# Performance work log

Hardware: AMD Instinct MI355X
Metric: run time of the kernel (lower is better)

## Reference

```python
import jax, jax.numpy as jnp
import numpy as np

N = 1_000_000   # active voxels
CIN = 32
COUT = 64
K = 9           # 3x3 kernel offsets (rulebook size)
EPS = 1e-5


def setup_inputs() -> dict:
    key = jax.random.key(0)
    ks = jax.random.split(key, 6)
    x = jax.random.normal(ks[0], (N, CIN), dtype=jnp.float32)
    # rulebook: neighbor index per (voxel, kernel offset); stride=1 so same coord set
    nbr = jax.random.randint(ks[1], (N, K), 0, N, dtype=jnp.int32)
    W1 = jax.random.normal(ks[2], (K, CIN, COUT), dtype=jnp.float32) * (1.0 / np.sqrt(K * CIN))
    W2 = jax.random.normal(ks[3], (K, COUT, COUT), dtype=jnp.float32) * (1.0 / np.sqrt(K * COUT))
    Wd = jax.random.normal(ks[4], (CIN, COUT), dtype=jnp.float32) * (1.0 / np.sqrt(CIN))
    g1 = jnp.ones((COUT,), jnp.float32); b1 = jnp.zeros((COUT,), jnp.float32)
    g2 = jnp.ones((COUT,), jnp.float32); b2 = jnp.zeros((COUT,), jnp.float32)
    gd = jnp.ones((COUT,), jnp.float32); bd = jnp.zeros((COUT,), jnp.float32)
    return {"x": x, "W1": W1, "g1": g1, "b1": b1, "W2": W2, "g2": g2, "b2": b2,
            "Wd": Wd, "gd": gd, "bd": bd, "nbr": nbr}


def _sparse_conv(x, nbr, W):
    # gather-GEMM-scatter; loop over the fixed K=9 kernel offsets to avoid
    # materializing the full [N, K, Cin] gathered tensor
    out = jnp.zeros((x.shape[0], W.shape[-1]), dtype=x.dtype)
    for k in range(W.shape[0]):
        out = out + jnp.take(x, nbr[:, k], axis=0) @ W[k]
    return out


def _bn(x, gamma, beta):
    # BatchNorm1d over the voxel dimension (training-mode batch statistics)
    mu = jnp.mean(x, axis=0)
    var = jnp.var(x, axis=0)
    return gamma * (x - mu) * jax.lax.rsqrt(var + EPS) + beta


def reference(x, W1, g1, b1, W2, g2, b2, Wd, gd, bd, nbr):
    # downsample branch (1x1 conv -> BN, no relu) since in_ch != out_ch
    identity = _bn(x @ Wd, gd, bd)
    # conv1: SparseConv3x3 -> BN -> ReLU
    out = jax.nn.relu(_bn(_sparse_conv(x, nbr, W1), g1, b1))
    # conv2: SparseConv3x3 -> BN (no relu)
    out = _bn(_sparse_conv(out, nbr, W2), g2, b2)
    # residual add + final ReLU
    return jax.nn.relu(out + identity)
```

## Files before the change

kernel.cpp:

```cpp
#include <hip/hip_runtime.h>
#include <hip/hip_bf16.h>

#define NV 1000000
#define CI 32
#define CO 64
#define KK 9
#define NG (NV / 16)
#define EPSV 1e-5f

typedef __bf16 bf16x8 __attribute__((ext_vector_type(8)));
typedef float  f32x4  __attribute__((ext_vector_type(4)));

__device__ __forceinline__ f32x4 mfma16(bf16x8 a, bf16x8 b, f32x4 c) {
    return __builtin_amdgcn_mfma_f32_16x16x32_bf16(a, b, c, 0, 0, 0);
}

__device__ __forceinline__ float xredseg(float v) {
    v += __shfl_xor(v, 16, 64);
    v += __shfl_xor(v, 32, 64);
    return v;
}

__global__ void k_prep_w(const float* __restrict__ W1, const float* __restrict__ W2,
                         const float* __restrict__ Wd,
                         __bf16* __restrict__ W1T, __bf16* __restrict__ W2T,
                         __bf16* __restrict__ WdT) {
    int i = blockIdx.x * blockDim.x + threadIdx.x;
    const int n1 = KK * CO * CI;
    const int n2 = KK * CO * CO;
    const int nd = CO * CI;
    if (i < n1) {
        int k = i / (CO * CI), r = i % (CO * CI), co = r / CI, ci = r % CI;
        W1T[i] = (__bf16)W1[(k * CI + ci) * CO + co];
    } else if (i < n1 + n2) {
        int j = i - n1;
        int k = j / (CO * CO), r = j % (CO * CO), co = r / CO, ci = r % CO;
        W2T[j] = (__bf16)W2[(k * CO + ci) * CO + co];
    } else if (i < n1 + n2 + nd) {
        int j = i - n1 - n2;
        int co = j / CI, ci = j % CI;
        WdT[j] = (__bf16)Wd[ci * CO + co];
    }
}

__global__ void k_prep_x(const float* __restrict__ x, __bf16* __restrict__ xb) {
    int i = blockIdx.x * blockDim.x + threadIdx.x;
    const float4* px = (const float4*)x + 2 * (size_t)i;
    float4 u = px[0], v = px[1];
    bf16x8 o;
    o[0] = (__bf16)u.x; o[1] = (__bf16)u.y; o[2] = (__bf16)u.z; o[3] = (__bf16)u.w;
    o[4] = (__bf16)v.x; o[5] = (__bf16)v.y; o[6] = (__bf16)v.z; o[7] = (__bf16)v.w;
    *((bf16x8*)xb + i) = o;
}

__global__ __launch_bounds__(256, 2) void k_conv1(
    const __bf16* __restrict__ xb, const int* __restrict__ nbr,
    const __bf16* __restrict__ W1T, const __bf16* __restrict__ WdT,
    __bf16* __restrict__ y1b, float* __restrict__ stats) {
    const int lane = threadIdx.x & 63;
    const int w    = threadIdx.x >> 6;
    const int r    = lane & 15;
    const int seg  = lane >> 4;

    bf16x8 w1[KK][4];
#pragma unroll
    for (int k = 0; k < KK; k++)
#pragma unroll
        for (int t = 0; t < 4; t++)
            w1[k][t] = *(const bf16x8*)(W1T + ((size_t)(k * CO + t * 16 + r)) * CI + seg * 8);
    bf16x8 wd[4];
#pragma unroll
    for (int t = 0; t < 4; t++)
        wd[t] = *(const bf16x8*)(WdT + (size_t)(t * 16 + r) * CI + seg * 8);

    float ps1[4] = {0.f,0.f,0.f,0.f}, pq1[4] = {0.f,0.f,0.f,0.f};
    float psd[4] = {0.f,0.f,0.f,0.f}, pqd[4] = {0.f,0.f,0.f,0.f};

    const int slot = blockIdx.x * 4 + w;
    const int nslots = gridDim.x * 4;
    const f32x4 z = {0.f, 0.f, 0.f, 0.f};

    for (int gid = slot; gid < NG; gid += nslots) {
        const int vb = gid * 16;
        const int v  = vb + r;
        const long nb = (long)v * KK;

        int idxs[KK];
#pragma unroll
        for (int k = 0; k < KK; k++) idxs[k] = nbr[nb + k];

        f32x4 acc[4]  = {z, z, z, z};
        f32x4 accd[4] = {z, z, z, z};

        bf16x8 ad = *(const bf16x8*)(xb + (size_t)v * CI + seg * 8);
#pragma unroll
        for (int t = 0; t < 4; t++) accd[t] = mfma16(ad, wd[t], accd[t]);

#pragma unroll
        for (int k = 0; k < KK; k++) {
            bf16x8 a = *(const bf16x8*)(xb + (size_t)idxs[k] * CI + seg * 8);
#pragma unroll
            for (int t = 0; t < 4; t++) acc[t] = mfma16(a, w1[k][t], acc[t]);
        }

#pragma unroll
        for (int t = 0; t < 4; t++) {
#pragma unroll
            for (int rr = 0; rr < 4; rr++) {
                float val = acc[t][rr];
                int row = vb + seg * 4 + rr;
                __builtin_nontemporal_store((__bf16)val, &y1b[(size_t)row * CO + t * 16 + r]);
                ps1[t] += val; pq1[t] += val * val;
                float dv = accd[t][rr];
                psd[t] += dv; pqd[t] += dv * dv;
            }
        }
    }

#pragma unroll
    for (int t = 0; t < 4; t++) {
        ps1[t] = xredseg(ps1[t]); pq1[t] = xredseg(pq1[t]);
        psd[t] = xredseg(psd[t]); pqd[t] = xredseg(pqd[t]);
    }
    if (lane < 16) {
#pragma unroll
        for (int t = 0; t < 4; t++) {
            atomicAdd(&stats[0 * 64 + t * 16 + lane], ps1[t]);
            atomicAdd(&stats[1 * 64 + t * 16 + lane], pq1[t]);
            atomicAdd(&stats[2 * 64 + t * 16 + lane], psd[t]);
            atomicAdd(&stats[3 * 64 + t * 16 + lane], pqd[t]);
        }
    }
}

__global__ void k_bnrelu(__bf16* __restrict__ y1b, const float* __restrict__ stats,
                         const float* __restrict__ g1, const float* __restrict__ b1) {
    __shared__ float sc[CO], sh[CO];
    int t = threadIdx.x;
    if (t < CO) {
        float mu  = stats[0 * 64 + t] * (1.0f / NV);
        float var = stats[1 * 64 + t] * (1.0f / NV) - mu * mu;
        float s = g1[t] * rsqrtf(var + EPSV);
        sc[t] = s; sh[t] = b1[t] - mu * s;
    }
    __syncthreads();
    size_t i = (size_t)blockIdx.x * blockDim.x + threadIdx.x;
    bf16x8* p = (bf16x8*)y1b + i;
    bf16x8 vv = *p;
    int c0 = 8 * ((int)(i & 7));
    bf16x8 o;
#pragma unroll
    for (int j = 0; j < 8; j++) {
        float f = (float)vv[j];
        f = sc[c0 + j] * f + sh[c0 + j];
        o[j] = (__bf16)fmaxf(f, 0.f);
    }
    *p = o;
}

#define TILE_B (16 * KK * 128)

__global__ __launch_bounds__(128, 2) void k_conv2(
    const __bf16* __restrict__ h1b, const int* __restrict__ nbr,
    const __bf16* __restrict__ W2T,
    float* __restrict__ y2, float* __restrict__ stats) {
    __shared__ __align__(16) char smem[2][TILE_B];

    const int lane = threadIdx.x & 63;
    const int w    = threadIdx.x >> 6;
    const int r    = lane & 15;
    const int seg  = lane >> 4;

    bf16x8 w2[KK][2][2];
#pragma unroll
    for (int k = 0; k < KK; k++)
#pragma unroll
        for (int t2 = 0; t2 < 2; t2++)
#pragma unroll
            for (int s = 0; s < 2; s++) {
                int co = w * 32 + t2 * 16 + r;
                int ci = s * 32 + seg * 8;
                w2[k][t2][s] = *(const bf16x8*)(W2T + ((size_t)(k * CO + co)) * CO + ci);
            }

    float ps[2] = {0.f, 0.f}, pq[2] = {0.f, 0.f};
    const f32x4 z = {0.f, 0.f, 0.f, 0.f};
    const int sw = r & 7;

    auto stage = [&](char* buf, int it) {
        const int* nb = nbr + (size_t)it * (16 * KK);
#pragma unroll
        for (int s = 0; s < 9; s++) {
            int c = w * 576 + s * 64 + lane;
            int ruleIdx = c >> 3;
            int i = (ruleIdx * 57) >> 9;
            int p = (c & 7) ^ (i & 7);
            int idx = nb[ruleIdx];
            const __bf16* src = h1b + (size_t)idx * CO + p * 8;
            __builtin_amdgcn_global_load_lds(
                (const __attribute__((address_space(1))) void*)src,
                (__attribute__((address_space(3))) void*)(buf + w * 9216 + s * 1024),
                16, 0, 0);
        }
    };

    int it = blockIdx.x;
    int cur = 0;
    if (it < NG) stage(smem[0], it);
    __syncthreads();

    for (; it < NG; it += gridDim.x) {
        int nxt = it + gridDim.x;
        if (nxt < NG) stage(smem[cur ^ 1], nxt);

        const __bf16* base = (const __bf16*)smem[cur];
        f32x4 acc[2] = {z, z};
#pragma unroll
        for (int k = 0; k < KK; k++) {
            const __bf16* rp = base + (size_t)(r * KK + k) * 64;
            bf16x8 a0 = *(const bf16x8*)(rp + ((seg ^ sw) * 8));
            bf16x8 a1 = *(const bf16x8*)(rp + (((4 + seg) ^ sw) * 8));
            acc[0] = mfma16(a0, w2[k][0][0], acc[0]);
            acc[0] = mfma16(a1, w2[k][0][1], acc[0]);
            acc[1] = mfma16(a0, w2[k][1][0], acc[1]);
            acc[1] = mfma16(a1, w2[k][1][1], acc[1]);
        }

        const int vb = it * 16;
#pragma unroll
        for (int t2 = 0; t2 < 2; t2++) {
#pragma unroll
            for (int rr = 0; rr < 4; rr++) {
                float val = acc[t2][rr];
                int row = vb + seg * 4 + rr;
                int c = w * 32 + t2 * 16 + r;
                __builtin_nontemporal_store(val, &y2[(size_t)row * CO + c]);
                ps[t2] += val; pq[t2] += val * val;
            }
        }

        __syncthreads();
        cur ^= 1;
    }

#pragma unroll
    for (int t2 = 0; t2 < 2; t2++) { ps[t2] = xredseg(ps[t2]); pq[t2] = xredseg(pq[t2]); }
    if (lane < 16) {
#pragma unroll
        for (int t2 = 0; t2 < 2; t2++) {
            atomicAdd(&stats[4 * 64 + w * 32 + t2 * 16 + lane], ps[t2]);
            atomicAdd(&stats[5 * 64 + w * 32 + t2 * 16 + lane], pq[t2]);
        }
    }
}

__global__ __launch_bounds__(256, 2) void k_final(
    const __bf16* __restrict__ xb, const __bf16* __restrict__ WdT,
    float* __restrict__ out, const float* __restrict__ stats,
    const float* __restrict__ g2, const float* __restrict__ b2,
    const float* __restrict__ gd, const float* __restrict__ bd) {
    __shared__ float s2[CO], sh2[CO], sdv[CO], shd[CO];
    int t = threadIdx.x;
    if (t < CO) {
        float mu2  = stats[4 * 64 + t] * (1.0f / NV);
        float var2 = stats[5 * 64 + t] * (1.0f / NV) - mu2 * mu2;
        float s = g2[t] * rsqrtf(var2 + EPSV);
        s2[t] = s; sh2[t] = b2[t] - mu2 * s;
        float mud  = stats[2 * 64 + t] * (1.0f / NV);
        float vard = stats[3 * 64 + t] * (1.0f / NV) - mud * mud;
        float sd = gd[t] * rsqrtf(vard + EPSV);
        sdv[t] = sd; shd[t] = bd[t] - mud * sd;
    }
    __syncthreads();

    const int lane = threadIdx.x & 63;
    const int w    = threadIdx.x >> 6;
    const int r    = lane & 15;
    const int seg  = lane >> 4;

    bf16x8 wd[4];
#pragma unroll
    for (int t4 = 0; t4 < 4; t4++)
        wd[t4] = *(const bf16x8*)(WdT + (size_t)(t4 * 16 + r) * CI + seg * 8);

    const int slot = blockIdx.x * 4 + w;
    const int nslots = gridDim.x * 4;
    const f32x4 z = {0.f, 0.f, 0.f, 0.f};

    for (int gid = slot; gid < NG; gid += nslots) {
        const int vb = gid * 16;
        const int v  = vb + r;
        bf16x8 ad = *(const bf16x8*)(xb + (size_t)v * CI + seg * 8);
        f32x4 accd[4] = {z, z, z, z};
#pragma unroll
        for (int t4 = 0; t4 < 4; t4++) accd[t4] = mfma16(ad, wd[t4], accd[t4]);
#pragma unroll
        for (int t4 = 0; t4 < 4; t4++) {
#pragma unroll
            for (int rr = 0; rr < 4; rr++) {
                int row = vb + seg * 4 + rr;
                int c = t4 * 16 + r;
                size_t o = (size_t)row * CO + c;
                float y2v = out[o];
                float res = s2[c] * y2v + sh2[c] + sdv[c] * accd[t4][rr] + shd[c];
                out[o] = fmaxf(res, 0.f);
            }
        }
    }
}

extern "C" void kernel_launch(void* const* d_in, const int* in_sizes, int n_in,
                              void* d_out, int out_size, void* d_ws, size_t ws_size,
                              hipStream_t stream) {
    const float* x  = (const float*)d_in[0];
    const float* W1 = (const float*)d_in[1];
    const float* g1 = (const float*)d_in[2];
    const float* b1 = (const float*)d_in[3];
    const float* W2 = (const float*)d_in[4];
    const float* g2 = (const float*)d_in[5];
    const float* b2 = (const float*)d_in[6];
    const float* Wd = (const float*)d_in[7];
    const float* gd = (const float*)d_in[8];
    const float* bd = (const float*)d_in[9];
    const int*  nbr = (const int*)d_in[10];

    char* ws = (char*)d_ws;
    __bf16* xb  = (__bf16*)ws;
    __bf16* y1b = (__bf16*)(ws + 64000000);
    __bf16* W1T = (__bf16*)(ws + 192000000);
    __bf16* W2T = W1T + KK * CO * CI;
    __bf16* WdT = W2T + KK * CO * CO;
    float* stats = (float*)(ws + 192000000 + 2 * (KK*CO*CI + KK*CO*CO + CO*CI));

    hipMemsetAsync(stats, 0, 6 * 64 * sizeof(float), stream);

    int nprep = KK*CO*CI + KK*CO*CO + CO*CI;
    k_prep_w<<<(nprep + 255) / 256, 256, 0, stream>>>(W1, W2, Wd, W1T, W2T, WdT);
    k_prep_x<<<(NV * CI / 8) / 256, 256, 0, stream>>>(x, xb);
    k_conv1<<<1024, 256, 0, stream>>>(xb, nbr, W1T, WdT, y1b, stats);
    k_bnrelu<<<(NV * CO / 8) / 256, 256, 0, stream>>>(y1b, stats, g1, b1);
    k_conv2<<<1024, 128, 0, stream>>>(y1b, nbr, W2T, (float*)d_out, stats);
    k_final<<<1024, 256, 0, stream>>>(xb, WdT, (float*)d_out, stats, g2, b2, gd, bd);
}
```

Baseline: 634.3 us.

## Double-buffer conv1 neighbor gathers into LDS with async global_load_lds

conv1 now gathers neighbor feature rows with asynchronous global-to-LDS loads into a per-wave double buffer. Neighbor indices for the next group are prefetched one step further ahead, and manual vmcnt waits replace the implicit dependency stalls. The goal is to overlap the random-access gather latency with the MFMA work on the current group. The kernel uses more LDS (about 72KB per block) and the grid is halved to 512 blocks. The hand-counted vmcnt thresholds make correctness depend on exactly how many memory instructions are in flight.

```diff
diff --git a/kernel.cpp b/kernel.cpp
--- a/kernel.cpp
+++ b/kernel.cpp
@@ -57,10 +57,14 @@
     const __bf16* __restrict__ xb, const int* __restrict__ nbr,
     const __bf16* __restrict__ W1T, const __bf16* __restrict__ WdT,
     __bf16* __restrict__ y1b, float* __restrict__ stats) {
+    __shared__ __align__(16) char smem[4][2][KK * 1024];
+
     const int lane = threadIdx.x & 63;
     const int w    = threadIdx.x >> 6;
     const int r    = lane & 15;
     const int seg  = lane >> 4;
+    const int rq   = lane >> 2;
+    const int part = lane & 3;
 
     bf16x8 w1[KK][4];
 #pragma unroll
@@ -76,29 +80,60 @@
     float ps1[4] = {0.f,0.f,0.f,0.f}, pq1[4] = {0.f,0.f,0.f,0.f};
     float psd[4] = {0.f,0.f,0.f,0.f}, pqd[4] = {0.f,0.f,0.f,0.f};
 
-    const int slot = blockIdx.x * 4 + w;
-    const int nslots = gridDim.x * 4;
+    const int slot   = blockIdx.x * 4 + w;
+    const int stride = gridDim.x * 4;
     const f32x4 z = {0.f, 0.f, 0.f, 0.f};
 
-    for (int gid = slot; gid < NG; gid += nslots) {
-        const int vb = gid * 16;
-        const int v  = vb + r;
-        const long nb = (long)v * KK;
-
-        int idxs[KK];
-#pragma unroll
-        for (int k = 0; k < KK; k++) idxs[k] = nbr[nb + k];
+    int idxs[KK];
+    auto load_idx = [&](int it) {
+        const volatile int* nb = nbr + (size_t)it * (16 * KK) + rq * KK;
+#pragma unroll
+        for (int k = 0; k < KK; k++) idxs[k] = nb[k];
+    };
+    auto stage = [&](int buf) {
+        char* dst = smem[w][buf];
+#pragma unroll
+        for (int k = 0; k < KK; k++) {
+            const __bf16* src = xb + (size_t)idxs[k] * CI + part * 8;
+            __builtin_amdgcn_global_load_lds(
+                (const __attribute__((address_space(1))) void*)src,
+                (__attribute__((address_space(3))) void*)(dst + k * 1024),
+                16, 0, 0);
+        }
+    };
+
+    int it  = slot;
+    load_idx(it);
+    stage(0);
+    int nxt = it + stride;
+    if (nxt < NG) load_idx(nxt);
+    int cur = 0;
+
+    while (true) {
+        const int nxt2 = nxt + stride;
+        if (nxt < NG) {
+            stage(cur ^ 1);
+            if (nxt2 < NG) load_idx(nxt2);
+        }
+        __builtin_amdgcn_sched_barrier(0);
+        if (nxt2 < NG)      asm volatile("s_waitcnt vmcnt(18)" ::: "memory");
+        else if (nxt < NG)  asm volatile("s_waitcnt vmcnt(9)"  ::: "memory");
+        else                asm volatile("s_waitcnt vmcnt(0)"  ::: "memory");
+        __builtin_amdgcn_sched_barrier(0);
+
+        const __bf16* base = (const __bf16*)smem[w][cur];
+        const int vb = it * 16;
 
         f32x4 acc[4]  = {z, z, z, z};
         f32x4 accd[4] = {z, z, z, z};
 
-        bf16x8 ad = *(const bf16x8*)(xb + (size_t)v * CI + seg * 8);
+        bf16x8 ad = *(const bf16x8*)(xb + (size_t)(vb + r) * CI + seg * 8);
 #pragma unroll
         for (int t = 0; t < 4; t++) accd[t] = mfma16(ad, wd[t], accd[t]);
 
 #pragma unroll
         for (int k = 0; k < KK; k++) {
-            bf16x8 a = *(const bf16x8*)(xb + (size_t)idxs[k] * CI + seg * 8);
+            bf16x8 a = *(const bf16x8*)(base + k * 512 + r * 32 + seg * 8);
 #pragma unroll
             for (int t = 0; t < 4; t++) acc[t] = mfma16(a, w1[k][t], acc[t]);
         }
@@ -115,6 +150,9 @@
                 psd[t] += dv; pqd[t] += dv * dv;
             }
         }
+
+        if (nxt >= NG) break;
+        it = nxt; nxt = nxt2; cur ^= 1;
     }
 
 #pragma unroll
@@ -337,7 +375,7 @@
     int nprep = KK*CO*CI + KK*CO*CO + CO*CI;
     k_prep_w<<<(nprep + 255) / 256, 256, 0, stream>>>(W1, W2, Wd, W1T, W2T, WdT);
     k_prep_x<<<(NV * CI / 8) / 256, 256, 0, stream>>>(x, xb);
-    k_conv1<<<1024, 256, 0, stream>>>(xb, nbr, W1T, WdT, y1b, stats);
+    k_conv1<<<512, 256, 0, stream>>>(xb, nbr, W1T, WdT, y1b, stats);
     k_bnrelu<<<(NV * CO / 8) / 256, 256, 0, stream>>>(y1b, stats, g1, b1);
     k_conv2<<<1024, 128, 0, stream>>>(y1b, nbr, W2T, (float*)d_out, stats);
     k_final<<<1024, 256, 0, stream>>>(xb, WdT, (float*)d_out, stats, g2, b2, gd, bd);
```

New measurement: 682.7 us. +7.6%, slower.

## Fuse BN+ReLU into conv2 gather and software-pipeline conv1 gathers with LDS weights

Applied to the files above, without the earlier changes.

Removes the separate BN+ReLU pass over y1 by applying the scale/shift and ReLU to each gathered neighbor row inside conv2 before the MFMA. This eliminates a full read and write of the intermediate, at the cost of repeating the elementwise work nine times per row in conv2. Conv1 now keeps W1 in LDS instead of registers and double-buffers the neighbor index loads and gathers across tiles to overlap memory latency with MFMA work. The conv1 grid is reduced to 768 blocks.

```diff
diff --git a/kernel.cpp b/kernel.cpp
--- a/kernel.cpp
+++ b/kernel.cpp
@@ -57,17 +57,23 @@
     const __bf16* __restrict__ xb, const int* __restrict__ nbr,
     const __bf16* __restrict__ W1T, const __bf16* __restrict__ WdT,
     __bf16* __restrict__ y1b, float* __restrict__ stats) {
+    __shared__ __align__(16) char w1smem[KK * CO * CI * 2];
+
     const int lane = threadIdx.x & 63;
     const int w    = threadIdx.x >> 6;
     const int r    = lane & 15;
     const int seg  = lane >> 4;
 
-    bf16x8 w1[KK][4];
-#pragma unroll
-    for (int k = 0; k < KK; k++)
-#pragma unroll
-        for (int t = 0; t < 4; t++)
-            w1[k][t] = *(const bf16x8*)(W1T + ((size_t)(k * CO + t * 16 + r)) * CI + seg * 8);
+#pragma unroll
+    for (int j = 0; j < 9; j++) {
+        const __bf16* srcp = W1T + (size_t)(j * 256 + threadIdx.x) * 8;
+        __builtin_amdgcn_global_load_lds(
+            (const __attribute__((address_space(1))) void*)srcp,
+            (__attribute__((address_space(3))) void*)(w1smem + j * 4096 + w * 1024),
+            16, 0, 0);
+    }
+    __syncthreads();
+
     bf16x8 wd[4];
 #pragma unroll
     for (int t = 0; t < 4; t++)
@@ -76,33 +82,42 @@
     float ps1[4] = {0.f,0.f,0.f,0.f}, pq1[4] = {0.f,0.f,0.f,0.f};
     float psd[4] = {0.f,0.f,0.f,0.f}, pqd[4] = {0.f,0.f,0.f,0.f};
 
-    const int slot = blockIdx.x * 4 + w;
-    const int nslots = gridDim.x * 4;
+    const int slot   = blockIdx.x * 4 + w;
+    const int stride = gridDim.x * 4;
     const f32x4 z = {0.f, 0.f, 0.f, 0.f};
 
-    for (int gid = slot; gid < NG; gid += nslots) {
-        const int vb = gid * 16;
-        const int v  = vb + r;
-        const long nb = (long)v * KK;
-
-        int idxs[KK];
-#pragma unroll
-        for (int k = 0; k < KK; k++) idxs[k] = nbr[nb + k];
+    auto loadIdx = [&](int (&idx)[KK], int tile) {
+        const int* nb = nbr + (size_t)(tile * 16 + r) * KK;
+#pragma unroll
+        for (int k = 0; k < KK; k++) idx[k] = nb[k];
+    };
+    auto gather9 = [&](bf16x8 (&g)[KK], const int (&idx)[KK]) {
+#pragma unroll
+        for (int k = 0; k < KK; k++)
+            g[k] = *(const bf16x8*)(xb + (size_t)idx[k] * CI + seg * 8);
+    };
+    auto loadAd = [&](int tile) {
+        return *(const bf16x8*)(xb + (size_t)(tile * 16 + r) * CI + seg * 8);
+    };
+    auto compute = [&](int tile, const bf16x8 (&g)[KK], bf16x8 ad) {
+        int w1off = 0;
+        asm volatile("" : "+v"(w1off));
+        const __bf16* wb = (const __bf16*)w1smem + w1off;
 
         f32x4 acc[4]  = {z, z, z, z};
         f32x4 accd[4] = {z, z, z, z};
-
-        bf16x8 ad = *(const bf16x8*)(xb + (size_t)v * CI + seg * 8);
 #pragma unroll
         for (int t = 0; t < 4; t++) accd[t] = mfma16(ad, wd[t], accd[t]);
-
 #pragma unroll
         for (int k = 0; k < KK; k++) {
-            bf16x8 a = *(const bf16x8*)(xb + (size_t)idxs[k] * CI + seg * 8);
-#pragma unroll
-            for (int t = 0; t < 4; t++) acc[t] = mfma16(a, w1[k][t], acc[t]);
-        }
-
+#pragma unroll
+            for (int t = 0; t < 4; t++) {
+                bf16x8 b = *(const bf16x8*)(wb + k * 2048 + t * 512 + r * 32 + seg * 8);
+                acc[t] = mfma16(g[k], b, acc[t]);
+            }
+        }
+
+        const int vb = tile * 16;
 #pragma unroll
         for (int t = 0; t < 4; t++) {
 #pragma unroll
@@ -115,6 +130,37 @@
                 psd[t] += dv; pqd[t] += dv * dv;
             }
         }
+    };
+
+    int idx0[KK], idx1[KK];
+    bf16x8 g0[KK], g1[KK];
+    bf16x8 ad0, ad1;
+
+    int it = slot;
+    loadIdx(idx0, it);
+    gather9(g0, idx0); ad0 = loadAd(it);
+    int itn = it + stride;
+    bool have = (itn < NG);
+    if (have) loadIdx(idx1, itn);
+
+    while (true) {
+        if (have) {
+            gather9(g1, idx1); ad1 = loadAd(itn);
+            int it2 = itn + stride;
+            if (it2 < NG) loadIdx(idx0, it2);
+        }
+        compute(it, g0, ad0);
+        if (!have) break;
+        it = itn; itn = it + stride; have = (itn < NG);
+
+        if (have) {
+            gather9(g0, idx0); ad0 = loadAd(itn);
+            int it2 = itn + stride;
+            if (it2 < NG) loadIdx(idx1, it2);
+        }
+        compute(it, g1, ad1);
+        if (!have) break;
+        it = itn; itn = it + stride; have = (itn < NG);
     }
 
 #pragma unroll
@@ -133,36 +179,12 @@
     }
 }
 
-__global__ void k_bnrelu(__bf16* __restrict__ y1b, const float* __restrict__ stats,
-                         const float* __restrict__ g1, const float* __restrict__ b1) {
-    __shared__ float sc[CO], sh[CO];
-    int t = threadIdx.x;
-    if (t < CO) {
-        float mu  = stats[0 * 64 + t] * (1.0f / NV);
-        float var = stats[1 * 64 + t] * (1.0f / NV) - mu * mu;
-        float s = g1[t] * rsqrtf(var + EPSV);
-        sc[t] = s; sh[t] = b1[t] - mu * s;
-    }
-    __syncthreads();
-    size_t i = (size_t)blockIdx.x * blockDim.x + threadIdx.x;
-    bf16x8* p = (bf16x8*)y1b + i;
-    bf16x8 vv = *p;
-    int c0 = 8 * ((int)(i & 7));
-    bf16x8 o;
-#pragma unroll
-    for (int j = 0; j < 8; j++) {
-        float f = (float)vv[j];
-        f = sc[c0 + j] * f + sh[c0 + j];
-        o[j] = (__bf16)fmaxf(f, 0.f);
-    }
-    *p = o;
-}
-
 #define TILE_B (16 * KK * 128)
 
 __global__ __launch_bounds__(128, 2) void k_conv2(
     const __bf16* __restrict__ h1b, const int* __restrict__ nbr,
-    const __bf16* __restrict__ W2T,
+    const __bf16* __restrict__ W2T, const float* __restrict__ g1,
+    const float* __restrict__ b1,
     float* __restrict__ y2, float* __restrict__ stats) {
     __shared__ __align__(16) char smem[2][TILE_B];
 
@@ -182,6 +204,21 @@
                 int ci = s * 32 + seg * 8;
                 w2[k][t2][s] = *(const bf16x8*)(W2T + ((size_t)(k * CO + co)) * CO + ci);
             }
+
+    float scA[8], shA[8], scB[8], shB[8];
+#pragma unroll
+    for (int j = 0; j < 8; j++) {
+        int cA = seg * 8 + j;
+        float muA = stats[cA] * (1.0f / NV);
+        float vaA = stats[64 + cA] * (1.0f / NV) - muA * muA;
+        float sA  = g1[cA] * rsqrtf(vaA + EPSV);
+        scA[j] = sA; shA[j] = b1[cA] - muA * sA;
+        int cB = 32 + seg * 8 + j;
+        float muB = stats[cB] * (1.0f / NV);
+        float vaB = stats[64 + cB] * (1.0f / NV) - muB * muB;
+        float sB  = g1[cB] * rsqrtf(vaB + EPSV);
+        scB[j] = sB; shB[j] = b1[cB] - muB * sB;
+    }
 
     float ps[2] = {0.f, 0.f}, pq[2] = {0.f, 0.f};
     const f32x4 z = {0.f, 0.f, 0.f, 0.f};
@@ -218,8 +255,14 @@
 #pragma unroll
         for (int k = 0; k < KK; k++) {
             const __bf16* rp = base + (size_t)(r * KK + k) * 64;
-            bf16x8 a0 = *(const bf16x8*)(rp + ((seg ^ sw) * 8));
-            bf16x8 a1 = *(const bf16x8*)(rp + (((4 + seg) ^ sw) * 8));
+            bf16x8 a0r = *(const bf16x8*)(rp + ((seg ^ sw) * 8));
+            bf16x8 a1r = *(const bf16x8*)(rp + (((4 + seg) ^ sw) * 8));
+            bf16x8 a0, a1;
+#pragma unroll
+            for (int j = 0; j < 8; j++) {
+                a0[j] = (__bf16)fmaxf((float)a0r[j] * scA[j] + shA[j], 0.f);
+                a1[j] = (__bf16)fmaxf((float)a1r[j] * scB[j] + shB[j], 0.f);
+            }
             acc[0] = mfma16(a0, w2[k][0][0], acc[0]);
             acc[0] = mfma16(a1, w2[k][0][1], acc[0]);
             acc[1] = mfma16(a0, w2[k][1][0], acc[1]);
@@ -337,8 +380,7 @@
     int nprep = KK*CO*CI + KK*CO*CO + CO*CI;
     k_prep_w<<<(nprep + 255) / 256, 256, 0, stream>>>(W1, W2, Wd, W1T, W2T, WdT);
     k_prep_x<<<(NV * CI / 8) / 256, 256, 0, stream>>>(x, xb);
-    k_conv1<<<1024, 256, 0, stream>>>(xb, nbr, W1T, WdT, y1b, stats);
-    k_bnrelu<<<(NV * CO / 8) / 256, 256, 0, stream>>>(y1b, stats, g1, b1);
-    k_conv2<<<1024, 128, 0, stream>>>(y1b, nbr, W2T, (float*)d_out, stats);
+    k_conv1<<<768, 256, 0, stream>>>(xb, nbr, W1T, WdT, y1b, stats);
+    k_conv2<<<1024, 128, 0, stream>>>(y1b, nbr, W2T, g1, b1, (float*)d_out, stats);
     k_final<<<1024, 256, 0, stream>>>(xb, WdT, (float*)d_out, stats, g2, b2, gd, bd);
 }
```

Result: faster. 601.8 us (-5.1%).
